# Optimization experiments

Measured on AMD Instinct MI355X. Metric: run time of the kernel, lower is better.

Reference implementation:

```python
import jax, jax.numpy as jnp
import numpy as np

N_NODES = 50000
N_EDGES = 800000
IN_DIM = 128
HID = 64
OUT_DIM = 128
N_GRAPHS = 128


def setup_inputs() -> dict:
    key = jax.random.key(0)
    ks = jax.random.split(key, 16)

    def lin(k, fan_in, fan_out):
        k1, k2 = jax.random.split(k)
        bound = 1.0 / np.sqrt(fan_in)
        W = jax.random.uniform(k1, (fan_in, fan_out), jnp.float32, -bound, bound)
        b = jax.random.uniform(k2, (fan_out,), jnp.float32, -bound, bound)
        return W, b

    x = jax.random.normal(ks[0], (N_NODES, IN_DIM), jnp.float32)
    edge_index = jax.random.randint(ks[1], (2, N_EDGES), 0, N_NODES, jnp.int64)
    batch = jnp.sort(jax.random.randint(ks[2], (N_NODES,), 0, N_GRAPHS, jnp.int64))

    W_in, b_in = lin(ks[3], IN_DIM, HID)
    W1_0, b1_0 = lin(ks[4], HID, HID)
    W2_0, b2_0 = lin(ks[5], HID, HID)
    W1_1, b1_1 = lin(ks[6], HID, HID)
    W2_1, b2_1 = lin(ks[7], HID, HID)
    W_out, b_out = lin(ks[8], HID, OUT_DIM)

    return dict(x=x, edge_index=edge_index, batch=batch,
                W_in=W_in, b_in=b_in,
                W1_0=W1_0, b1_0=b1_0, W2_0=W2_0, b2_0=b2_0,
                W1_1=W1_1, b1_1=b1_1, W2_1=W2_1, b2_1=b2_1,
                W_out=W_out, b_out=b_out)


def _gin_conv(x, src, dst, W1, b1, W2, b2):
    # aggr[i] = sum_{(s,i) in E} x[s]; GIN (eps=0): h = MLP(x + aggr)
    msgs = x[src]  # [E, HID] gather
    aggr = jax.ops.segment_sum(msgs, dst, num_segments=N_NODES)
    h = x + aggr
    h = jax.nn.relu(h @ W1 + b1)
    return h @ W2 + b2


def reference(x, edge_index, batch,
              W_in, b_in,
              W1_0, b1_0, W2_0, b2_0,
              W1_1, b1_1, W2_1, b2_1,
              W_out, b_out):
    src, dst = edge_index[0], edge_index[1]
    h = x @ W_in + b_in  # proj_in
    # conv 0 (+ReLU; dropout is identity in eval mode)
    h = jax.nn.relu(_gin_conv(h, src, dst, W1_0, b1_0, W2_0, b2_0))
    # conv 1
    h = jax.nn.relu(_gin_conv(h, src, dst, W1_1, b1_1, W2_1, b2_1))
    h = h @ W_out + b_out  # proj_out -> [N, OUT_DIM]
    # global mean pool over graphs
    sums = jax.ops.segment_sum(h, batch, num_segments=N_GRAPHS)
    counts = jax.ops.segment_sum(jnp.ones((h.shape[0],), h.dtype), batch, num_segments=N_GRAPHS)
    graph_emb = sums / jnp.maximum(counts, 1.0)[:, None]  # [N_GRAPHS, OUT_DIM]
    return graph_emb
```

## Files before the change

### kernel.cpp

```cpp
#include <hip/hip_runtime.h>
#include <hip/hip_fp16.h>

#define N_NODES   50000
#define N_EDGES   800000
#define IN_DIM    128
#define HID       64
#define OUT_DIM   128
#define N_GRAPHS  128

#define NBKT      196
#define BBLK      392
#define BSTRIDE   5120
#define CAP       42

#define OFF_GCUR   0
#define OFF_GSUM   196
#define OFF_GSTART 8388
#define OFF_ROWPTR 8518
#define OFF_SRCL   58520
#define OFF_EPAIRS 458520
#define OFF_HA     1462040
#define OFF_HB     2262040
#define OFF_WT     3062040

typedef float v2f __attribute__((ext_vector_type(2)));
typedef float f32x4 __attribute__((ext_vector_type(4)));
typedef short bf16x8 __attribute__((ext_vector_type(8)));

union FragU { uint4 u; bf16x8 v; };

__device__ __forceinline__ unsigned short f2bf(float f) {
    union { float f; unsigned int u; } v; v.f = f;
    const unsigned int r = v.u + 0x7FFFu + ((v.u >> 16) & 1u);
    return (unsigned short)(r >> 16);
}

__device__ __forceinline__ void acc_fp8x8(float acc[8], const uint2 w) {
    const v2f a = __builtin_amdgcn_cvt_pk_f32_fp8(w.x, false);
    const v2f b = __builtin_amdgcn_cvt_pk_f32_fp8(w.x, true);
    const v2f c = __builtin_amdgcn_cvt_pk_f32_fp8(w.y, false);
    const v2f d = __builtin_amdgcn_cvt_pk_f32_fp8(w.y, true);
    acc[0] += a.x; acc[1] += a.y; acc[2] += b.x; acc[3] += b.y;
    acc[4] += c.x; acc[5] += c.y; acc[6] += d.x; acc[7] += d.y;
}

__device__ __forceinline__ uint2 pack_fp8x8(const float f[8]) {
    int w0 = 0, w1 = 0;
    w0 = __builtin_amdgcn_cvt_pk_fp8_f32(f[0], f[1], w0, false);
    w0 = __builtin_amdgcn_cvt_pk_fp8_f32(f[2], f[3], w0, true);
    w1 = __builtin_amdgcn_cvt_pk_fp8_f32(f[4], f[5], w1, false);
    w1 = __builtin_amdgcn_cvt_pk_fp8_f32(f[6], f[7], w1, true);
    uint2 r; r.x = (unsigned)w0; r.y = (unsigned)w1;
    return r;
}

#define K1_SMEM_BYTES 34816

__device__ __forceinline__ void role_bucket(char* smem, const int* __restrict__ ei,
                                            int* __restrict__ gcur,
                                            unsigned int* __restrict__ epairs,
                                            int bid) {
    int* lcnt = (int*)smem;
    unsigned int* stage = (unsigned int*)(smem + NBKT * 4);
    const int t = threadIdx.x;
    for (int i = t; i < NBKT; i += 256) lcnt[i] = 0;
    __syncthreads();
    for (int e0 = bid * 512; e0 < N_EDGES; e0 += BBLK * 512) {
#pragma unroll
        for (int half = 0; half < 2; ++half) {
            const int e = e0 + half * 256 + t;
            if (e < N_EDGES) {
                const unsigned int src = (unsigned int)ei[e];
                const unsigned int dst = (unsigned int)ei[N_EDGES + e];
                const int b = dst >> 8;
                const unsigned int pk = src | (dst << 16);
                const int pos = atomicAdd(&lcnt[b], 1);
                if (pos < CAP) stage[b * CAP + pos] = pk;
                else {
                    const int gp = atomicAdd(&gcur[b], 1);
                    epairs[b * BSTRIDE + gp] = pk;
                }
            }
        }
    }
    __syncthreads();
    if (t < NBKT) {
        int n = lcnt[t]; if (n > CAP) n = CAP;
        if (n > 0) {
            const int base = atomicAdd(&gcur[t], n);
            for (int i = 0; i < n; ++i)
                epairs[t * BSTRIDE + base + i] = stage[t * CAP + i];
        }
    }
}

__device__ __forceinline__ void role_gbound(const int* __restrict__ batch,
                                            int* __restrict__ gstart, int bid) {
    const int n = bid * 256 + threadIdx.x;
    if (n >= N_NODES) return;
    const int b = batch[n];
    if (n == 0) {
        for (int g = 0; g <= b; ++g) gstart[g] = 0;
    } else {
        const int p = batch[n - 1];
        for (int g = p + 1; g <= b; ++g) gstart[g] = n;
    }
    if (n == N_NODES - 1) {
        for (int g = b + 1; g <= N_GRAPHS; ++g) gstart[g] = N_NODES;
    }
}

__device__ __forceinline__ void role_wprep(const float* __restrict__ W10,
                                           const float* __restrict__ W20,
                                           const float* __restrict__ W11,
                                           const float* __restrict__ W21,
                                           unsigned short* __restrict__ wtg) {
    const int t = threadIdx.x;
    const float* Ws[4] = {W10, W20, W11, W21};
#pragma unroll
    for (int m = 0; m < 4; ++m) {
        unsigned short* o = wtg + 8704 + m * 4608;
        const float* w = Ws[m];
        for (int i = t; i < 64 * 64; i += 256) {
            const int k = i >> 6, c = i & 63;
            o[c * 72 + k] = f2bf(w[i]);
        }
    }
}

__device__ __forceinline__ void role_proj(char* smem, const float* __restrict__ x,
                                          const float* __restrict__ Wi,
                                          const float* __restrict__ b,
                                          unsigned char* __restrict__ h8, int bid) {
    unsigned short* X16 = (unsigned short*)smem;
    unsigned short* Wt  = (unsigned short*)(smem + 17408);
    float* OUT32 = (float*)smem;
    const int t = threadIdx.x;
    const int nb = bid * 64;
    for (int i = t; i < 128 * 64; i += 256) {
        const int k = i >> 6, c = i & 63;
        Wt[c * 136 + k] = f2bf(Wi[i]);
    }
    for (int i = t; i < 64 * (IN_DIM / 4); i += 256) {
        const int n = i >> 5;
        const int k4 = (i & 31) * 4;
        float4 val = make_float4(0.f, 0.f, 0.f, 0.f);
        if (nb + n < N_NODES)
            val = *(const float4*)(x + (size_t)(nb + n) * IN_DIM + k4);
        union { uint2 u; unsigned short s[4]; } pk;
        pk.s[0] = f2bf(val.x); pk.s[1] = f2bf(val.y);
        pk.s[2] = f2bf(val.z); pk.s[3] = f2bf(val.w);
        *(uint2*)&X16[n * 136 + k4] = pk.u;
    }
    __syncthreads();

    const int l = t & 63;
    const int m0 = (t >> 6) * 16;
    const int lrow = l & 15;
    const int lk = (l >> 4) * 8;
    FragU a[4];
#pragma unroll
    for (int s = 0; s < 4; ++s)
        a[s].u = *(const uint4*)&X16[(m0 + lrow) * 136 + s * 32 + lk];
    f32x4 acc[4];
#pragma unroll
    for (int n = 0; n < 4; ++n) {
        const float bv = b[n * 16 + lrow];
        acc[n] = (f32x4){bv, bv, bv, bv};
#pragma unroll
        for (int s = 0; s < 4; ++s) {
            FragU w;
            w.u = *(const uint4*)&Wt[(n * 16 + lrow) * 136 + s * 32 + lk];
            acc[n] = __builtin_amdgcn_mfma_f32_16x16x32_bf16(a[s].v, w.v, acc[n], 0, 0, 0);
        }
    }
    __syncthreads();
#pragma unroll
    for (int n = 0; n < 4; ++n)
#pragma unroll
        for (int r = 0; r < 4; ++r)
            OUT32[(m0 + (l >> 4) * 4 + r) * 68 + n * 16 + lrow] = acc[n][r];
    __syncthreads();
    const int ln = t & 31;
    const int c0 = (t >> 5) * 8;
#pragma unroll
    for (int j = 0; j < 2; ++j) {
        const int n = nb + ln + 32 * j;
        if (n < N_NODES) {
            float f[8];
            const float* src = &OUT32[(ln + 32 * j) * 68 + c0];
            *(float4*)&f[0] = *(const float4*)&src[0];
            *(float4*)&f[4] = *(const float4*)&src[4];
            const uint2 p = pack_fp8x8(f);
            *(uint2*)(h8 + (size_t)n * HID + c0) = p;
        }
    }
}

__global__ __launch_bounds__(256) void k_bg(
        const int* __restrict__ ei, const int* __restrict__ batch,
        int* __restrict__ gcur, unsigned int* __restrict__ epairs,
        int* __restrict__ gstart,
        const float* __restrict__ x, const float* __restrict__ Wi,
        const float* __restrict__ bi, unsigned char* __restrict__ hA,
        const float* __restrict__ W10, const float* __restrict__ W20,
        const float* __restrict__ W11, const float* __restrict__ W21,
        unsigned short* __restrict__ wtg) {
    __shared__ __attribute__((aligned(16))) char smem[K1_SMEM_BYTES];
    const int bid = blockIdx.x;
    if (bid < BBLK)                   role_bucket(smem, ei, gcur, epairs, bid);
    else if (bid < BBLK + NBKT)       role_gbound(batch, gstart, bid - BBLK);
    else if (bid == BBLK + NBKT)      role_wprep(W10, W20, W11, W21, wtg);
    else                              role_proj(smem, x, Wi, bi, hA, bid - (BBLK + NBKT + 1));
}

#define CSR_SMEM_BYTES 22560

__global__ __launch_bounds__(256) void k_csr(
        const int* __restrict__ gcur, const unsigned int* __restrict__ epairs,
        int* __restrict__ rowptr, unsigned short* __restrict__ srclist) {
    __shared__ __attribute__((aligned(16))) char smem[CSR_SMEM_BYTES];
    int* lhist = (int*)smem;
    int* lcur  = lhist + 256;
    int* pws   = lcur + 256;
    int* wtot  = pws + 4;
    int* lsrc  = wtot + 4;
    const int b = blockIdx.x;
    const int t = threadIdx.x;
    const int lane = t & 63, wv = t >> 6;

    int po = 0;
    for (int j = t; j < b; j += 256) po += gcur[j];
#pragma unroll
    for (int m = 32; m; m >>= 1) po += __shfl_xor(po, m, 64);
    if (lane == 0) pws[wv] = po;
    lhist[t] = 0;
    __syncthreads();
    const int base = pws[0] + pws[1] + pws[2] + pws[3];
    const int cnt = gcur[b];

    for (int i = t; i < cnt; i += 256)
        atomicAdd(&lhist[(epairs[b * BSTRIDE + i] >> 16) & 255], 1);
    __syncthreads();

    const int d = lhist[t];
    int incl = d;
#pragma unroll
    for (int off = 1; off < 64; off <<= 1) {
        const int u = __shfl_up(incl, off, 64);
        if (lane >= off) incl += u;
    }
    if (lane == 63) wtot[wv] = incl;
    __syncthreads();
    int woff = 0;
#pragma unroll
    for (int i = 0; i < 4; ++i) woff += (i < wv) ? wtot[i] : 0;
    const int excl = woff + incl - d;
    lcur[t] = excl;
    const int node = b * 256 + t;
    if (node < N_NODES) rowptr[node] = base + excl;
    if (b == NBKT - 1 && t == 0) rowptr[N_NODES] = base + cnt;
    __syncthreads();

    for (int i = t; i < cnt; i += 256) {
        const unsigned int u = epairs[b * BSTRIDE + i];
        const int pos = atomicAdd(&lcur[(u >> 16) & 255], 1);
        lsrc[pos] = (int)(u & 0xFFFFu);
    }
    __syncthreads();
    for (int i = t; i < cnt; i += 256)
        srclist[base + i] = (unsigned short)lsrc[i];
}

#define S_AB 72
template<int POOL>
__global__ __launch_bounds__(256, 4) void k_conv_t(
        const unsigned char* __restrict__ hin8,
        const int* __restrict__ rowptr, const unsigned short* __restrict__ srclist,
        const unsigned short* __restrict__ W1t_g, const float* __restrict__ b1,
        const unsigned short* __restrict__ W2t_g, const float* __restrict__ b2,
        unsigned char* __restrict__ hout8,
        const int* __restrict__ batch, float* __restrict__ gsum) {
    __shared__ __attribute__((aligned(16))) char csm[36864];
    unsigned short* A16 = (unsigned short*)csm;
    unsigned short* H16 = (unsigned short*)(csm + 9216);
    unsigned short* W1t = (unsigned short*)(csm + 18432);
    unsigned short* W2t = (unsigned short*)(csm + 27648);
    float* OUT32 = (float*)csm;
    const int t = threadIdx.x;
    {
        const uint4* s1 = (const uint4*)W1t_g;
        const uint4* s2 = (const uint4*)W2t_g;
        uint4* d1 = (uint4*)W1t;
        uint4* d2 = (uint4*)W2t;
        for (int i = t; i < 576; i += 256) { d1[i] = s1[i]; d2[i] = s2[i]; }
    }

    const int nb = blockIdx.x * 64;
    const int grp = t >> 3;
    const int q = t & 7;
#pragma unroll
    for (int pass = 0; pass < 2; ++pass) {
        const int nloc = pass * 32 + grp;
        const int node = nb + nloc;
        float acc[8] = {0.f, 0.f, 0.f, 0.f, 0.f, 0.f, 0.f, 0.f};
        if (node < N_NODES) {
            acc_fp8x8(acc, *(const uint2*)(hin8 + (size_t)node * HID + q * 8));
            const int beg = rowptr[node];
            const int end = rowptr[node + 1];
            int e = beg;
            for (; e + 8 <= end; e += 8) {
                int s[8];
#pragma unroll
                for (int i = 0; i < 8; ++i) s[i] = srclist[e + i];
                uint2 r[8];
#pragma unroll
                for (int i = 0; i < 8; ++i)
                    r[i] = *(const uint2*)(hin8 + (size_t)s[i] * HID + q * 8);
#pragma unroll
                for (int i = 0; i < 8; ++i) acc_fp8x8(acc, r[i]);
            }
            for (; e < end; ++e)
                acc_fp8x8(acc, *(const uint2*)(hin8 + (size_t)srclist[e] * HID + q * 8));
        }
        union { uint4 u; unsigned short s[8]; } ou;
#pragma unroll
        for (int c = 0; c < 8; ++c) ou.s[c] = f2bf(acc[c]);
        *(uint4*)&A16[nloc * S_AB + q * 8] = ou.u;
    }
    __syncthreads();

    const int l = t & 63;
    const int m0 = (t >> 6) * 16;
    const int lrow = l & 15;
    const int lk = (l >> 4) * 8;

    FragU a0, a1;
    a0.u = *(const uint4*)&A16[(m0 + lrow) * S_AB + lk];
    a1.u = *(const uint4*)&A16[(m0 + lrow) * S_AB + 32 + lk];
    f32x4 acc1[4];
#pragma unroll
    for (int n = 0; n < 4; ++n) {
        const float bv = b1[n * 16 + lrow];
        acc1[n] = (f32x4){bv, bv, bv, bv};
        FragU w0, w1;
        w0.u = *(const uint4*)&W1t[(n * 16 + lrow) * S_AB + lk];
        w1.u = *(const uint4*)&W1t[(n * 16 + lrow) * S_AB + 32 + lk];
        acc1[n] = __builtin_amdgcn_mfma_f32_16x16x32_bf16(a0.v, w0.v, acc1[n], 0, 0, 0);
        acc1[n] = __builtin_amdgcn_mfma_f32_16x16x32_bf16(a1.v, w1.v, acc1[n], 0, 0, 0);
    }
    __syncthreads();
#pragma unroll
    for (int n = 0; n < 4; ++n)
#pragma unroll
        for (int r = 0; r < 4; ++r) {
            const int row = m0 + (l >> 4) * 4 + r;
            H16[row * S_AB + n * 16 + lrow] = f2bf(fmaxf(acc1[n][r], 0.0f));
        }
    __syncthreads();

    FragU h0, h1;
    h0.u = *(const uint4*)&H16[(m0 + lrow) * S_AB + lk];
    h1.u = *(const uint4*)&H16[(m0 + lrow) * S_AB + 32 + lk];
    f32x4 acc2[4];
#pragma unroll
    for (int n = 0; n < 4; ++n) {
        const float bv = b2[n * 16 + lrow];
        acc2[n] = (f32x4){bv, bv, bv, bv};
        FragU w0, w1;
        w0.u = *(const uint4*)&W2t[(n * 16 + lrow) * S_AB + lk];
        w1.u = *(const uint4*)&W2t[(n * 16 + lrow) * S_AB + 32 + lk];
        acc2[n] = __builtin_amdgcn_mfma_f32_16x16x32_bf16(h0.v, w0.v, acc2[n], 0, 0, 0);
        acc2[n] = __builtin_amdgcn_mfma_f32_16x16x32_bf16(h1.v, w1.v, acc2[n], 0, 0, 0);
    }
    __syncthreads();
#pragma unroll
    for (int n = 0; n < 4; ++n)
#pragma unroll
        for (int r = 0; r < 4; ++r)
            OUT32[(m0 + (l >> 4) * 4 + r) * 68 + n * 16 + lrow] = fmaxf(acc2[n][r], 0.0f);
    __syncthreads();

    const int ln = t & 31;
    const int c0 = (t >> 5) * 8;
    if constexpr (POOL) {
        const int nlast = (nb + 64 <= N_NODES) ? nb + 63 : N_NODES - 1;
        const int g0 = batch[nb];
        const int g1 = batch[nlast];
        int myg[2];
        float f[2][8];
#pragma unroll
        for (int j = 0; j < 2; ++j) {
            const int n = nb + ln + 32 * j;
            myg[j] = (n < N_NODES) ? batch[n] : -1;
            const float* src = &OUT32[(ln + 32 * j) * 68 + c0];
            *(float4*)&f[j][0] = *(const float4*)&src[0];
            *(float4*)&f[j][4] = *(const float4*)&src[4];
        }
        for (int g = g0; g <= g1; ++g) {
#pragma unroll
            for (int j = 0; j < 2; ++j) {
#pragma unroll
                for (int c = 0; c < 8; ++c) {
                    float v = (myg[j] == g) ? f[j][c] : 0.0f;
#pragma unroll
                    for (int m = 16; m; m >>= 1) v += __shfl_xor(v, m, 64);
                    if (ln == 0) atomicAdd(&gsum[g * HID + c0 + c], v);
                }
            }
        }
    } else {
#pragma unroll
        for (int j = 0; j < 2; ++j) {
            const int n = nb + ln + 32 * j;
            if (n < N_NODES) {
                float f[8];
                const float* src = &OUT32[(ln + 32 * j) * 68 + c0];
                *(float4*)&f[0] = *(const float4*)&src[0];
                *(float4*)&f[4] = *(const float4*)&src[4];
                const uint2 p = pack_fp8x8(f);
                *(uint2*)(hout8 + (size_t)n * HID + c0) = p;
            }
        }
    }
}

__global__ __launch_bounds__(128) void k_out(
        const float* __restrict__ gsum, const int* __restrict__ gstart,
        const float* __restrict__ Wo, const float* __restrict__ bo,
        float* __restrict__ out) {
    __shared__ float mean[HID];
    const int g = blockIdx.x;
    const int t = threadIdx.x;
    const int cnt = gstart[g + 1] - gstart[g];
    if (t < HID)
        mean[t] = (cnt > 0) ? gsum[g * HID + t] / (float)cnt : 0.0f;
    __syncthreads();
    float o = 0.0f;
    for (int k = 0; k < HID; ++k)
        o = fmaf(mean[k], Wo[k * OUT_DIM + t], o);
    out[g * OUT_DIM + t] = (cnt > 0) ? o + bo[t] : 0.0f;
}

extern "C" void kernel_launch(void* const* d_in, const int* in_sizes, int n_in,
                              void* d_out, int out_size, void* d_ws, size_t ws_size,
                              hipStream_t stream) {
    const float* x     = (const float*)d_in[0];
    const int*   ei    = (const int*)d_in[1];
    const int*   batch = (const int*)d_in[2];
    const float* W_in  = (const float*)d_in[3];
    const float* b_in  = (const float*)d_in[4];
    const float* W1_0  = (const float*)d_in[5];
    const float* b1_0  = (const float*)d_in[6];
    const float* W2_0  = (const float*)d_in[7];
    const float* b2_0  = (const float*)d_in[8];
    const float* W1_1  = (const float*)d_in[9];
    const float* b1_1  = (const float*)d_in[10];
    const float* W2_1  = (const float*)d_in[11];
    const float* b2_1  = (const float*)d_in[12];
    const float* W_out = (const float*)d_in[13];
    const float* b_out = (const float*)d_in[14];
    float* out = (float*)d_out;

    unsigned int*   wsw    = (unsigned int*)d_ws;
    int*            gcur   = (int*)(wsw + OFF_GCUR);
    float*          gsum   = (float*)(wsw + OFF_GSUM);
    int*            gstart = (int*)(wsw + OFF_GSTART);
    int*            rowptr = (int*)(wsw + OFF_ROWPTR);
    unsigned short* srcl   = (unsigned short*)(wsw + OFF_SRCL);
    unsigned int*   epairs = (unsigned int*)(wsw + OFF_EPAIRS);
    unsigned char*  hA     = (unsigned char*)(wsw + OFF_HA);
    unsigned char*  hB     = (unsigned char*)(wsw + OFF_HB);
    unsigned short* wtg    = (unsigned short*)(wsw + OFF_WT);

    unsigned short* wt10  = wtg + 8704;
    unsigned short* wt20  = wtg + 13312;
    unsigned short* wt11  = wtg + 17920;
    unsigned short* wt21  = wtg + 22528;

    const int pi_blocks = (N_NODES + 63) / 64;
    const int cv_blocks = (N_NODES + 63) / 64;
    const int bg_blocks = BBLK + NBKT + 1 + pi_blocks;

    hipMemsetAsync(gcur, 0, (NBKT + N_GRAPHS * HID) * sizeof(int), stream);
    k_bg<<<bg_blocks, 256, 0, stream>>>(ei, batch, gcur, epairs, gstart,
                                        x, W_in, b_in, hA,
                                        W1_0, W2_0, W1_1, W2_1, wtg);
    k_csr<<<NBKT, 256, 0, stream>>>(gcur, epairs, rowptr, srcl);
    k_conv_t<0><<<cv_blocks, 256, 0, stream>>>(hA, rowptr, srcl,
                                               wt10, b1_0, wt20, b2_0, hB,
                                               batch, gsum);
    k_conv_t<1><<<cv_blocks, 256, 0, stream>>>(hB, rowptr, srcl,
                                               wt11, b1_1, wt21, b2_1, hA,
                                               batch, gsum);
    k_out<<<N_GRAPHS, 128, 0, stream>>>(gsum, gstart, W_out, b_out, out);
}
```

Baseline: 175.3 us.

## Pad CSR rows to multiples of eight with dummy node, interleave two-node gathers

Measured after the change: 186.8 us. +6.5%, slower.

```diff
diff --git a/kernel.cpp b/kernel.cpp
--- a/kernel.cpp
+++ b/kernel.cpp
@@ -12,16 +12,16 @@
 #define BBLK      392
 #define BSTRIDE   5120
 #define CAP       42
+#define SRCSTRIDE 10240
 
 #define OFF_GCUR   0
 #define OFF_GSUM   196
 #define OFF_GSTART 8388
 #define OFF_ROWPTR 8518
-#define OFF_SRCL   58520
 #define OFF_EPAIRS 458520
 #define OFF_HA     1462040
-#define OFF_HB     2262040
-#define OFF_WT     3062040
+#define OFF_HB     2262056
+#define OFF_WT     3062072
 
 typedef float v2f __attribute__((ext_vector_type(2)));
 typedef float f32x4 __attribute__((ext_vector_type(4)));
@@ -52,6 +52,41 @@
     w1 = __builtin_amdgcn_cvt_pk_fp8_f32(f[6], f[7], w1, true);
     uint2 r; r.x = (unsigned)w0; r.y = (unsigned)w1;
     return r;
+}
+
+__global__ __launch_bounds__(256) void k_prep(
+        const float* __restrict__ Wi,
+        const float* __restrict__ W10, const float* __restrict__ W20,
+        const float* __restrict__ W11, const float* __restrict__ W21,
+        unsigned short* __restrict__ wtg, int* __restrict__ gcur,
+        float* __restrict__ gsum,
+        unsigned char* __restrict__ hA, unsigned char* __restrict__ hB) {
+    __shared__ float L[128 * 64];
+    const int b = blockIdx.x, t = threadIdx.x;
+    if (b == 0) {
+        for (int i = t; i < 128 * 64; i += 256) L[i] = Wi[i];
+        __syncthreads();
+        for (int i = t; i < 64 * 136; i += 256) {
+            const int c = i / 136, k = i - c * 136;
+            wtg[i] = (k < 128) ? f2bf(L[k * 64 + c]) : (unsigned short)0;
+        }
+    } else if (b <= 4) {
+        const float* W = (b == 1) ? W10 : (b == 2) ? W20 : (b == 3) ? W11 : W21;
+        for (int i = t; i < 64 * 64; i += 256) L[i] = W[i];
+        __syncthreads();
+        unsigned short* o = wtg + 8704 + (b - 1) * 4608;
+        for (int i = t; i < 64 * 72; i += 256) {
+            const int c = i / 72, k = i - c * 72;
+            o[i] = (k < 64) ? f2bf(L[k * 64 + c]) : (unsigned short)0;
+        }
+    } else {
+        for (int i = t; i < NBKT; i += 256) gcur[i] = 0;
+        for (int i = t; i < N_GRAPHS * HID; i += 256) gsum[i] = 0.0f;
+        if (t < 16) {
+            ((unsigned int*)(hA + (size_t)N_NODES * HID))[t] = 0u;
+            ((unsigned int*)(hB + (size_t)N_NODES * HID))[t] = 0u;
+        }
+    }
 }
 
 #define K1_SMEM_BYTES 34816
@@ -110,26 +145,8 @@
     }
 }
 
-__device__ __forceinline__ void role_wprep(const float* __restrict__ W10,
-                                           const float* __restrict__ W20,
-                                           const float* __restrict__ W11,
-                                           const float* __restrict__ W21,
-                                           unsigned short* __restrict__ wtg) {
-    const int t = threadIdx.x;
-    const float* Ws[4] = {W10, W20, W11, W21};
-#pragma unroll
-    for (int m = 0; m < 4; ++m) {
-        unsigned short* o = wtg + 8704 + m * 4608;
-        const float* w = Ws[m];
-        for (int i = t; i < 64 * 64; i += 256) {
-            const int k = i >> 6, c = i & 63;
-            o[c * 72 + k] = f2bf(w[i]);
-        }
-    }
-}
-
 __device__ __forceinline__ void role_proj(char* smem, const float* __restrict__ x,
-                                          const float* __restrict__ Wi,
+                                          const unsigned short* __restrict__ Wt_g,
                                           const float* __restrict__ b,
                                           unsigned char* __restrict__ h8, int bid) {
     unsigned short* X16 = (unsigned short*)smem;
@@ -137,9 +154,10 @@
     float* OUT32 = (float*)smem;
     const int t = threadIdx.x;
     const int nb = bid * 64;
-    for (int i = t; i < 128 * 64; i += 256) {
-        const int k = i >> 6, c = i & 63;
-        Wt[c * 136 + k] = f2bf(Wi[i]);
+    {
+        const uint4* s = (const uint4*)Wt_g;
+        uint4* d = (uint4*)Wt;
+        for (int i = t; i < 1088; i += 256) d[i] = s[i];
     }
     for (int i = t; i < 64 * (IN_DIM / 4); i += 256) {
         const int n = i >> 5;
@@ -201,42 +219,27 @@
         const int* __restrict__ ei, const int* __restrict__ batch,
         int* __restrict__ gcur, unsigned int* __restrict__ epairs,
         int* __restrict__ gstart,
-        const float* __restrict__ x, const float* __restrict__ Wi,
-        const float* __restrict__ bi, unsigned char* __restrict__ hA,
-        const float* __restrict__ W10, const float* __restrict__ W20,
-        const float* __restrict__ W11, const float* __restrict__ W21,
-        unsigned short* __restrict__ wtg) {
+        const float* __restrict__ x, const unsigned short* __restrict__ wt_in,
+        const float* __restrict__ bi, unsigned char* __restrict__ hA) {
     __shared__ __attribute__((aligned(16))) char smem[K1_SMEM_BYTES];
     const int bid = blockIdx.x;
-    if (bid < BBLK)                   role_bucket(smem, ei, gcur, epairs, bid);
-    else if (bid < BBLK + NBKT)       role_gbound(batch, gstart, bid - BBLK);
-    else if (bid == BBLK + NBKT)      role_wprep(W10, W20, W11, W21, wtg);
-    else                              role_proj(smem, x, Wi, bi, hA, bid - (BBLK + NBKT + 1));
-}
-
-#define CSR_SMEM_BYTES 22560
+    if (bid < BBLK)              role_bucket(smem, ei, gcur, epairs, bid);
+    else if (bid < BBLK + NBKT)  role_gbound(batch, gstart, bid - BBLK);
+    else                         role_proj(smem, x, wt_in, bi, hA, bid - (BBLK + NBKT));
+}
 
 __global__ __launch_bounds__(256) void k_csr(
         const int* __restrict__ gcur, const unsigned int* __restrict__ epairs,
-        int* __restrict__ rowptr, unsigned short* __restrict__ srclist) {
-    __shared__ __attribute__((aligned(16))) char smem[CSR_SMEM_BYTES];
-    int* lhist = (int*)smem;
-    int* lcur  = lhist + 256;
-    int* pws   = lcur + 256;
-    int* wtot  = pws + 4;
-    int* lsrc  = wtot + 4;
+        int* __restrict__ rowptr2, unsigned short* __restrict__ srclist) {
+    __shared__ int lhist[256];
+    __shared__ int lcur[256];
+    __shared__ int wtot[4];
+    __shared__ int lsrc[8192];
     const int b = blockIdx.x;
     const int t = threadIdx.x;
     const int lane = t & 63, wv = t >> 6;
-
-    int po = 0;
-    for (int j = t; j < b; j += 256) po += gcur[j];
-#pragma unroll
-    for (int m = 32; m; m >>= 1) po += __shfl_xor(po, m, 64);
-    if (lane == 0) pws[wv] = po;
     lhist[t] = 0;
     __syncthreads();
-    const int base = pws[0] + pws[1] + pws[2] + pws[3];
     const int cnt = gcur[b];
 
     for (int i = t; i < cnt; i += 256)
@@ -244,7 +247,8 @@
     __syncthreads();
 
     const int d = lhist[t];
-    int incl = d;
+    const int p8 = (d + 7) & ~7;
+    int incl = p8;
 #pragma unroll
     for (int off = 1; off < 64; off <<= 1) {
         const int u = __shfl_up(incl, off, 64);
@@ -255,78 +259,92 @@
     int woff = 0;
 #pragma unroll
     for (int i = 0; i < 4; ++i) woff += (i < wv) ? wtot[i] : 0;
-    const int excl = woff + incl - d;
-    lcur[t] = excl;
+    const int exclP = woff + incl - p8;
+    lcur[t] = exclP;
     const int node = b * 256 + t;
-    if (node < N_NODES) rowptr[node] = base + excl;
-    if (b == NBKT - 1 && t == 0) rowptr[N_NODES] = base + cnt;
-    __syncthreads();
-
+    if (node < N_NODES) rowptr2[node] = (b * SRCSTRIDE + exclP) | ((p8 >> 3) << 24);
+    __syncthreads();
+    const int padTot = wtot[0] + wtot[1] + wtot[2] + wtot[3];
+    for (int i = t; i < padTot; i += 256) lsrc[i] = N_NODES;
+    __syncthreads();
     for (int i = t; i < cnt; i += 256) {
         const unsigned int u = epairs[b * BSTRIDE + i];
         const int pos = atomicAdd(&lcur[(u >> 16) & 255], 1);
         lsrc[pos] = (int)(u & 0xFFFFu);
     }
     __syncthreads();
-    for (int i = t; i < cnt; i += 256)
-        srclist[base + i] = (unsigned short)lsrc[i];
+    for (int i = t; i < padTot; i += 256)
+        srclist[b * SRCSTRIDE + i] = (unsigned short)lsrc[i];
 }
 
 #define S_AB 72
+
+__device__ __forceinline__ void gather8(float acc[8],
+                                        const unsigned char* __restrict__ hin8,
+                                        const uint4 c, const int q) {
+    unsigned s[8] = {c.x & 0xFFFFu, c.x >> 16, c.y & 0xFFFFu, c.y >> 16,
+                     c.z & 0xFFFFu, c.z >> 16, c.w & 0xFFFFu, c.w >> 16};
+    uint2 r[8];
+#pragma unroll
+    for (int j = 0; j < 8; ++j)
+        r[j] = *(const uint2*)(hin8 + (size_t)s[j] * HID + q * 8);
+#pragma unroll
+    for (int j = 0; j < 8; ++j) acc_fp8x8(acc, r[j]);
+}
+
 template<int POOL>
-__global__ __launch_bounds__(256, 4) void k_conv_t(
+__global__ __launch_bounds__(256, 5) void k_conv_t(
         const unsigned char* __restrict__ hin8,
-        const int* __restrict__ rowptr, const unsigned short* __restrict__ srclist,
+        const int* __restrict__ rowptr2, const unsigned short* __restrict__ srclist,
         const unsigned short* __restrict__ W1t_g, const float* __restrict__ b1,
         const unsigned short* __restrict__ W2t_g, const float* __restrict__ b2,
         unsigned char* __restrict__ hout8,
         const int* __restrict__ batch, float* __restrict__ gsum) {
-    __shared__ __attribute__((aligned(16))) char csm[36864];
+    __shared__ __attribute__((aligned(16))) char csm[27648];
     unsigned short* A16 = (unsigned short*)csm;
     unsigned short* H16 = (unsigned short*)(csm + 9216);
-    unsigned short* W1t = (unsigned short*)(csm + 18432);
-    unsigned short* W2t = (unsigned short*)(csm + 27648);
+    unsigned short* Wt  = (unsigned short*)(csm + 18432);
     float* OUT32 = (float*)csm;
     const int t = threadIdx.x;
     {
         const uint4* s1 = (const uint4*)W1t_g;
-        const uint4* s2 = (const uint4*)W2t_g;
-        uint4* d1 = (uint4*)W1t;
-        uint4* d2 = (uint4*)W2t;
-        for (int i = t; i < 576; i += 256) { d1[i] = s1[i]; d2[i] = s2[i]; }
+        uint4* d1 = (uint4*)Wt;
+        for (int i = t; i < 576; i += 256) d1[i] = s1[i];
     }
 
     const int nb = blockIdx.x * 64;
     const int grp = t >> 3;
     const int q = t & 7;
-#pragma unroll
-    for (int pass = 0; pass < 2; ++pass) {
-        const int nloc = pass * 32 + grp;
-        const int node = nb + nloc;
-        float acc[8] = {0.f, 0.f, 0.f, 0.f, 0.f, 0.f, 0.f, 0.f};
-        if (node < N_NODES) {
-            acc_fp8x8(acc, *(const uint2*)(hin8 + (size_t)node * HID + q * 8));
-            const int beg = rowptr[node];
-            const int end = rowptr[node + 1];
-            int e = beg;
-            for (; e + 8 <= end; e += 8) {
-                int s[8];
-#pragma unroll
-                for (int i = 0; i < 8; ++i) s[i] = srclist[e + i];
-                uint2 r[8];
-#pragma unroll
-                for (int i = 0; i < 8; ++i)
-                    r[i] = *(const uint2*)(hin8 + (size_t)s[i] * HID + q * 8);
-#pragma unroll
-                for (int i = 0; i < 8; ++i) acc_fp8x8(acc, r[i]);
-            }
-            for (; e < end; ++e)
-                acc_fp8x8(acc, *(const uint2*)(hin8 + (size_t)srclist[e] * HID + q * 8));
-        }
-        union { uint4 u; unsigned short s[8]; } ou;
-#pragma unroll
-        for (int c = 0; c < 8; ++c) ou.s[c] = f2bf(acc[c]);
-        *(uint4*)&A16[nloc * S_AB + q * 8] = ou.u;
+    const int nA = nb + grp;
+    const int nB = nb + 32 + grp;
+    float accA[8] = {0,0,0,0,0,0,0,0};
+    float accB[8] = {0,0,0,0,0,0,0,0};
+    int begA = 0, chA = 0, begB = 0, chB = 0;
+    if (nA < N_NODES) {
+        const int v = rowptr2[nA]; begA = v & 0xFFFFFF; chA = v >> 24;
+        acc_fp8x8(accA, *(const uint2*)(hin8 + (size_t)nA * HID + q * 8));
+    }
+    if (nB < N_NODES) {
+        const int v = rowptr2[nB]; begB = v & 0xFFFFFF; chB = v >> 24;
+        acc_fp8x8(accB, *(const uint2*)(hin8 + (size_t)nB * HID + q * 8));
+    }
+    const int iters = chA > chB ? chA : chB;
+    uint4 iA = {0,0,0,0}, iB = {0,0,0,0};
+    if (chA) iA = *(const uint4*)&srclist[begA];
+    if (chB) iB = *(const uint4*)&srclist[begB];
+    for (int i = 0; i < iters; ++i) {
+        const uint4 cA = iA, cB = iB;
+        if (i + 1 < chA) iA = *(const uint4*)&srclist[begA + (i + 1) * 8];
+        if (i + 1 < chB) iB = *(const uint4*)&srclist[begB + (i + 1) * 8];
+        if (i < chA) gather8(accA, hin8, cA, q);
+        if (i < chB) gather8(accB, hin8, cB, q);
+    }
+    {
+        union { uint4 u; unsigned short s[8]; } oa, ob;
+#pragma unroll
+        for (int c = 0; c < 8; ++c) { oa.s[c] = f2bf(accA[c]); ob.s[c] = f2bf(accB[c]); }
+        *(uint4*)&A16[grp * S_AB + q * 8] = oa.u;
+        *(uint4*)&A16[(grp + 32) * S_AB + q * 8] = ob.u;
     }
     __syncthreads();
 
@@ -344,8 +362,8 @@
         const float bv = b1[n * 16 + lrow];
         acc1[n] = (f32x4){bv, bv, bv, bv};
         FragU w0, w1;
-        w0.u = *(const uint4*)&W1t[(n * 16 + lrow) * S_AB + lk];
-        w1.u = *(const uint4*)&W1t[(n * 16 + lrow) * S_AB + 32 + lk];
+        w0.u = *(const uint4*)&Wt[(n * 16 + lrow) * S_AB + lk];
+        w1.u = *(const uint4*)&Wt[(n * 16 + lrow) * S_AB + 32 + lk];
         acc1[n] = __builtin_amdgcn_mfma_f32_16x16x32_bf16(a0.v, w0.v, acc1[n], 0, 0, 0);
         acc1[n] = __builtin_amdgcn_mfma_f32_16x16x32_bf16(a1.v, w1.v, acc1[n], 0, 0, 0);
     }
@@ -357,6 +375,11 @@
             const int row = m0 + (l >> 4) * 4 + r;
             H16[row * S_AB + n * 16 + lrow] = f2bf(fmaxf(acc1[n][r], 0.0f));
         }
+    {
+        const uint4* s2 = (const uint4*)W2t_g;
+        uint4* d2 = (uint4*)Wt;
+        for (int i = t; i < 576; i += 256) d2[i] = s2[i];
+    }
     __syncthreads();
 
     FragU h0, h1;
@@ -368,8 +391,8 @@
         const float bv = b2[n * 16 + lrow];
         acc2[n] = (f32x4){bv, bv, bv, bv};
         FragU w0, w1;
-        w0.u = *(const uint4*)&W2t[(n * 16 + lrow) * S_AB + lk];
-        w1.u = *(const uint4*)&W2t[(n * 16 + lrow) * S_AB + 32 + lk];
+        w0.u = *(const uint4*)&Wt[(n * 16 + lrow) * S_AB + lk];
+        w1.u = *(const uint4*)&Wt[(n * 16 + lrow) * S_AB + 32 + lk];
         acc2[n] = __builtin_amdgcn_mfma_f32_16x16x32_bf16(h0.v, w0.v, acc2[n], 0, 0, 0);
         acc2[n] = __builtin_amdgcn_mfma_f32_16x16x32_bf16(h1.v, w1.v, acc2[n], 0, 0, 0);
     }
@@ -467,12 +490,13 @@
     float*          gsum   = (float*)(wsw + OFF_GSUM);
     int*            gstart = (int*)(wsw + OFF_GSTART);
     int*            rowptr = (int*)(wsw + OFF_ROWPTR);
-    unsigned short* srcl   = (unsigned short*)(wsw + OFF_SRCL);
     unsigned int*   epairs = (unsigned int*)(wsw + OFF_EPAIRS);
+    unsigned short* srcl   = (unsigned short*)(wsw + OFF_EPAIRS);
     unsigned char*  hA     = (unsigned char*)(wsw + OFF_HA);
     unsigned char*  hB     = (unsigned char*)(wsw + OFF_HB);
     unsigned short* wtg    = (unsigned short*)(wsw + OFF_WT);
 
+    unsigned short* wt_in = wtg;
     unsigned short* wt10  = wtg + 8704;
     unsigned short* wt20  = wtg + 13312;
     unsigned short* wt11  = wtg + 17920;
@@ -480,12 +504,12 @@
 
     const int pi_blocks = (N_NODES + 63) / 64;
     const int cv_blocks = (N_NODES + 63) / 64;
-    const int bg_blocks = BBLK + NBKT + 1 + pi_blocks;
-
-    hipMemsetAsync(gcur, 0, (NBKT + N_GRAPHS * HID) * sizeof(int), stream);
+    const int bg_blocks = BBLK + NBKT + pi_blocks;
+
+    k_prep<<<6, 256, 0, stream>>>(W_in, W1_0, W2_0, W1_1, W2_1,
+                                  wtg, gcur, gsum, hA, hB);
     k_bg<<<bg_blocks, 256, 0, stream>>>(ei, batch, gcur, epairs, gstart,
-                                        x, W_in, b_in, hA,
-                                        W1_0, W2_0, W1_1, W2_1, wtg);
+                                        x, wt_in, b_in, hA);
     k_csr<<<NBKT, 256, 0, stream>>>(gcur, epairs, rowptr, srcl);
     k_conv_t<0><<<cv_blocks, 256, 0, stream>>>(hA, rowptr, srcl,
                                                wt10, b1_0, wt20, b2_0, hB,
```

## Pad per-node edge lists to multiples of eight with a zero dummy row

Applied to the files above, without the earlier changes.

Result: faster. 170.0 us (-3.1%).

```diff
diff --git a/kernel.cpp b/kernel.cpp
--- a/kernel.cpp
+++ b/kernel.cpp
@@ -12,16 +12,16 @@
 #define BBLK      392
 #define BSTRIDE   5120
 #define CAP       42
+#define SRCSTRIDE 10240
 
 #define OFF_GCUR   0
 #define OFF_GSUM   196
 #define OFF_GSTART 8388
 #define OFF_ROWPTR 8518
-#define OFF_SRCL   58520
 #define OFF_EPAIRS 458520
 #define OFF_HA     1462040
-#define OFF_HB     2262040
-#define OFF_WT     3062040
+#define OFF_HB     2262056
+#define OFF_WT     3062072
 
 typedef float v2f __attribute__((ext_vector_type(2)));
 typedef float f32x4 __attribute__((ext_vector_type(4)));
@@ -114,7 +114,9 @@
                                            const float* __restrict__ W20,
                                            const float* __restrict__ W11,
                                            const float* __restrict__ W21,
-                                           unsigned short* __restrict__ wtg) {
+                                           unsigned short* __restrict__ wtg,
+                                           unsigned char* __restrict__ hA,
+                                           unsigned char* __restrict__ hB) {
     const int t = threadIdx.x;
     const float* Ws[4] = {W10, W20, W11, W21};
 #pragma unroll
@@ -125,6 +127,10 @@
             const int k = i >> 6, c = i & 63;
             o[c * 72 + k] = f2bf(w[i]);
         }
+    }
+    if (t < 16) {
+        ((unsigned int*)(hA + (size_t)N_NODES * HID))[t] = 0u;
+        ((unsigned int*)(hB + (size_t)N_NODES * HID))[t] = 0u;
     }
 }
 
@@ -203,40 +209,30 @@
         int* __restrict__ gstart,
         const float* __restrict__ x, const float* __restrict__ Wi,
         const float* __restrict__ bi, unsigned char* __restrict__ hA,
+        unsigned char* __restrict__ hB,
         const float* __restrict__ W10, const float* __restrict__ W20,
         const float* __restrict__ W11, const float* __restrict__ W21,
         unsigned short* __restrict__ wtg) {
     __shared__ __attribute__((aligned(16))) char smem[K1_SMEM_BYTES];
     const int bid = blockIdx.x;
-    if (bid < BBLK)                   role_bucket(smem, ei, gcur, epairs, bid);
-    else if (bid < BBLK + NBKT)       role_gbound(batch, gstart, bid - BBLK);
-    else if (bid == BBLK + NBKT)      role_wprep(W10, W20, W11, W21, wtg);
-    else                              role_proj(smem, x, Wi, bi, hA, bid - (BBLK + NBKT + 1));
-}
-
-#define CSR_SMEM_BYTES 22560
+    if (bid < BBLK)              role_bucket(smem, ei, gcur, epairs, bid);
+    else if (bid < BBLK + NBKT)  role_gbound(batch, gstart, bid - BBLK);
+    else if (bid == BBLK + NBKT) role_wprep(W10, W20, W11, W21, wtg, hA, hB);
+    else                         role_proj(smem, x, Wi, bi, hA, bid - (BBLK + NBKT + 1));
+}
 
 __global__ __launch_bounds__(256) void k_csr(
         const int* __restrict__ gcur, const unsigned int* __restrict__ epairs,
-        int* __restrict__ rowptr, unsigned short* __restrict__ srclist) {
-    __shared__ __attribute__((aligned(16))) char smem[CSR_SMEM_BYTES];
-    int* lhist = (int*)smem;
-    int* lcur  = lhist + 256;
-    int* pws   = lcur + 256;
-    int* wtot  = pws + 4;
-    int* lsrc  = wtot + 4;
+        int* __restrict__ rowptr2, unsigned short* __restrict__ srclist) {
+    __shared__ int lhist[256];
+    __shared__ int lcur[256];
+    __shared__ int wtot[4];
+    __shared__ int lsrc[8192];
     const int b = blockIdx.x;
     const int t = threadIdx.x;
     const int lane = t & 63, wv = t >> 6;
-
-    int po = 0;
-    for (int j = t; j < b; j += 256) po += gcur[j];
-#pragma unroll
-    for (int m = 32; m; m >>= 1) po += __shfl_xor(po, m, 64);
-    if (lane == 0) pws[wv] = po;
     lhist[t] = 0;
     __syncthreads();
-    const int base = pws[0] + pws[1] + pws[2] + pws[3];
     const int cnt = gcur[b];
 
     for (int i = t; i < cnt; i += 256)
@@ -244,7 +240,8 @@
     __syncthreads();
 
     const int d = lhist[t];
-    int incl = d;
+    const int p8 = (d + 7) & ~7;
+    int incl = p8;
 #pragma unroll
     for (int off = 1; off < 64; off <<= 1) {
         const int u = __shfl_up(incl, off, 64);
@@ -255,28 +252,43 @@
     int woff = 0;
 #pragma unroll
     for (int i = 0; i < 4; ++i) woff += (i < wv) ? wtot[i] : 0;
-    const int excl = woff + incl - d;
-    lcur[t] = excl;
+    const int exclP = woff + incl - p8;
+    lcur[t] = exclP;
     const int node = b * 256 + t;
-    if (node < N_NODES) rowptr[node] = base + excl;
-    if (b == NBKT - 1 && t == 0) rowptr[N_NODES] = base + cnt;
-    __syncthreads();
-
+    if (node < N_NODES) rowptr2[node] = (b * SRCSTRIDE + exclP) | ((p8 >> 3) << 24);
+    __syncthreads();
+    const int padTot = wtot[0] + wtot[1] + wtot[2] + wtot[3];
+    for (int i = t; i < padTot; i += 256) lsrc[i] = N_NODES;
+    __syncthreads();
     for (int i = t; i < cnt; i += 256) {
         const unsigned int u = epairs[b * BSTRIDE + i];
         const int pos = atomicAdd(&lcur[(u >> 16) & 255], 1);
         lsrc[pos] = (int)(u & 0xFFFFu);
     }
     __syncthreads();
-    for (int i = t; i < cnt; i += 256)
-        srclist[base + i] = (unsigned short)lsrc[i];
+    for (int i = t; i < padTot; i += 256)
+        srclist[b * SRCSTRIDE + i] = (unsigned short)lsrc[i];
 }
 
 #define S_AB 72
+
+__device__ __forceinline__ void gather8(float acc[8],
+                                        const unsigned char* __restrict__ hin8,
+                                        const uint4 c, const int q) {
+    unsigned s[8] = {c.x & 0xFFFFu, c.x >> 16, c.y & 0xFFFFu, c.y >> 16,
+                     c.z & 0xFFFFu, c.z >> 16, c.w & 0xFFFFu, c.w >> 16};
+    uint2 r[8];
+#pragma unroll
+    for (int j = 0; j < 8; ++j)
+        r[j] = *(const uint2*)(hin8 + (size_t)s[j] * HID + q * 8);
+#pragma unroll
+    for (int j = 0; j < 8; ++j) acc_fp8x8(acc, r[j]);
+}
+
 template<int POOL>
 __global__ __launch_bounds__(256, 4) void k_conv_t(
         const unsigned char* __restrict__ hin8,
-        const int* __restrict__ rowptr, const unsigned short* __restrict__ srclist,
+        const int* __restrict__ rowptr2, const unsigned short* __restrict__ srclist,
         const unsigned short* __restrict__ W1t_g, const float* __restrict__ b1,
         const unsigned short* __restrict__ W2t_g, const float* __restrict__ b2,
         unsigned char* __restrict__ hout8,
@@ -306,22 +318,17 @@
         float acc[8] = {0.f, 0.f, 0.f, 0.f, 0.f, 0.f, 0.f, 0.f};
         if (node < N_NODES) {
             acc_fp8x8(acc, *(const uint2*)(hin8 + (size_t)node * HID + q * 8));
-            const int beg = rowptr[node];
-            const int end = rowptr[node + 1];
-            int e = beg;
-            for (; e + 8 <= end; e += 8) {
-                int s[8];
-#pragma unroll
-                for (int i = 0; i < 8; ++i) s[i] = srclist[e + i];
-                uint2 r[8];
-#pragma unroll
-                for (int i = 0; i < 8; ++i)
-                    r[i] = *(const uint2*)(hin8 + (size_t)s[i] * HID + q * 8);
-#pragma unroll
-                for (int i = 0; i < 8; ++i) acc_fp8x8(acc, r[i]);
+            const int v = rowptr2[node];
+            const int beg = v & 0xFFFFFF;
+            const int ch = (int)((unsigned)v >> 24);
+            if (ch) {
+                uint4 idx = *(const uint4*)&srclist[beg];
+                for (int i = 0; i < ch; ++i) {
+                    const uint4 cur = idx;
+                    if (i + 1 < ch) idx = *(const uint4*)&srclist[beg + (i + 1) * 8];
+                    gather8(acc, hin8, cur, q);
+                }
             }
-            for (; e < end; ++e)
-                acc_fp8x8(acc, *(const uint2*)(hin8 + (size_t)srclist[e] * HID + q * 8));
         }
         union { uint4 u; unsigned short s[8]; } ou;
 #pragma unroll
@@ -467,8 +474,8 @@
     float*          gsum   = (float*)(wsw + OFF_GSUM);
     int*            gstart = (int*)(wsw + OFF_GSTART);
     int*            rowptr = (int*)(wsw + OFF_ROWPTR);
-    unsigned short* srcl   = (unsigned short*)(wsw + OFF_SRCL);
     unsigned int*   epairs = (unsigned int*)(wsw + OFF_EPAIRS);
+    unsigned short* srcl   = (unsigned short*)(wsw + OFF_EPAIRS);
     unsigned char*  hA     = (unsigned char*)(wsw + OFF_HA);
     unsigned char*  hB     = (unsigned char*)(wsw + OFF_HB);
     unsigned short* wtg    = (unsigned short*)(wsw + OFF_WT);
@@ -484,7 +491,7 @@
 
     hipMemsetAsync(gcur, 0, (NBKT + N_GRAPHS * HID) * sizeof(int), stream);
     k_bg<<<bg_blocks, 256, 0, stream>>>(ei, batch, gcur, epairs, gstart,
-                                        x, W_in, b_in, hA,
+                                        x, W_in, b_in, hA, hB,
                                         W1_0, W2_0, W1_1, W2_1, wtg);
     k_csr<<<NBKT, 256, 0, stream>>>(gcur, epairs, rowptr, srcl);
     k_conv_t<0><<<cv_blocks, 256, 0, stream>>>(hA, rowptr, srcl,
```
